# Kernel optimization log

Hardware: AMD Instinct MI355X
Metric: run time of the kernel (lower is better)

The kernel has to match this reference:

```python
import jax, jax.numpy as jnp
import numpy as np

B, X, Y, Z = 2, 64, 64, 48
T_IN, T_OUT = 10, 20
WIDTH = 20
G = 4              # number of fields / groups
M1 = M2 = M3 = 8   # fourier modes
L = 4              # layers
ORDER = [[0, 1, 2, 3], [1, 2, 3, 0], [2, 3, 0, 1], [3, 0, 1, 2]]
CIN = WIDTH * 4    # mWidth_input_parameters[i] == 4
COUT = WIDTH       # nWidth_output_parameters[i] == 1
EPS = 1e-5


def setup_inputs() -> dict:
    key = jax.random.key(0)
    ks = jax.random.split(key, 12)
    s = 0.02
    return {
        "x": jax.random.normal(ks[0], (B, X, Y, Z, G * T_IN), jnp.float32),
        "p_w": jax.random.normal(ks[1], (G, T_IN + 3, WIDTH), jnp.float32) * s,
        "p_b": jnp.zeros((G, WIDTH), jnp.float32),
        # complex spectral weights stored as (..., 2) = (real, imag); 4 corner blocks
        "spec_w": jax.random.normal(ks[2], (L, G, 4, CIN, COUT, M1, M2, M3, 2), jnp.float32) * (1.0 / CIN),
        "mlp_w1": jax.random.normal(ks[3], (L, G, COUT, COUT), jnp.float32) * s,
        "mlp_b1": jnp.zeros((L, G, COUT), jnp.float32),
        "mlp_w2": jax.random.normal(ks[4], (L, G, COUT, COUT), jnp.float32) * s,
        "mlp_b2": jnp.zeros((L, G, COUT), jnp.float32),
        "w_w": jax.random.normal(ks[5], (L, G, COUT, CIN), jnp.float32) * s,
        "w_b": jnp.zeros((L, G, COUT), jnp.float32),
        "q_w1": jax.random.normal(ks[6], (G, 4 * COUT, COUT), jnp.float32) * s,
        "q_b1": jnp.zeros((G, 4 * COUT), jnp.float32),
        "q_w2": jax.random.normal(ks[7], (G, T_OUT, 4 * COUT), jnp.float32) * s,
        "q_b2": jnp.zeros((G, T_OUT), jnp.float32),
    }


def _instance_norm(v):  # (B,C,X,Y,Z); InstanceNorm3d, affine=False
    m = v.mean(axis=(-3, -2, -1), keepdims=True)
    var = v.var(axis=(-3, -2, -1), keepdims=True)
    return (v - m) * jax.lax.rsqrt(var + EPS)


def _conv1x1(v, w, b):  # w: (Co, Ci)
    return jnp.einsum('bixyz,oi->boxyz', v, w) + b[None, :, None, None, None]


def _gelu(v):
    return jax.nn.gelu(v, approximate=False)


def _spectral(v, w):  # v: (B,Ci,X,Y,Z); w: complex (4,Ci,Co,M1,M2,M3)
    ft = jnp.fft.rfftn(v, axes=(-3, -2, -1))
    mul = lambda xc, wc: jnp.einsum('bixyz,ioxyz->boxyz', xc, wc)
    out = jnp.zeros((v.shape[0], w.shape[2], X, Y, Z // 2 + 1), ft.dtype)
    out = out.at[:, :, :M1, :M2, :M3].set(mul(ft[:, :, :M1, :M2, :M3], w[0]))
    out = out.at[:, :, -M1:, :M2, :M3].set(mul(ft[:, :, -M1:, :M2, :M3], w[1]))
    out = out.at[:, :, :M1, -M2:, :M3].set(mul(ft[:, :, :M1, -M2:, :M3], w[2]))
    out = out.at[:, :, -M1:, -M2:, :M3].set(mul(ft[:, :, -M1:, -M2:, :M3], w[3]))
    return jnp.fft.irfftn(out, s=(X, Y, Z), axes=(-3, -2, -1))


def _grid():  # (1,X,Y,Z,3), linspace 0..1 per axis
    gx = jnp.linspace(0.0, 1.0, X, dtype=jnp.float32)[:, None, None]
    gy = jnp.linspace(0.0, 1.0, Y, dtype=jnp.float32)[None, :, None]
    gz = jnp.linspace(0.0, 1.0, Z, dtype=jnp.float32)[None, None, :]
    g = jnp.stack([jnp.broadcast_to(gx, (X, Y, Z)),
                   jnp.broadcast_to(gy, (X, Y, Z)),
                   jnp.broadcast_to(gz, (X, Y, Z))], axis=-1)
    return g[None]


def reference(x, p_w, p_b, spec_w, mlp_w1, mlp_b1, mlp_w2, mlp_b2,
              w_w, w_b, q_w1, q_b1, q_w2, q_b2):
    grid = jnp.broadcast_to(_grid(), (x.shape[0], X, Y, Z, 3))
    # --- lifting: per-field Linear(T_in+3 -> width) ---
    lifted = [jnp.concatenate([x[..., i * T_IN:(i + 1) * T_IN], grid], axis=-1) @ p_w[i] + p_b[i]
              for i in range(G)]
    h = jnp.concatenate(lifted, axis=-1).transpose(0, 4, 1, 2, 3)  # (B, width*G, X, Y, Z)
    sw = spec_w[..., 0] + 1j * spec_w[..., 1]
    for l in range(L):
        for i in range(G):
            # faithful gather quirk: first index duplicated, last index dropped
            idx = [ORDER[i][0]] + ORDER[i][:-1]
            xg = jnp.concatenate([h[:, WIDTH * k:WIDTH * (k + 1)] for k in idx], axis=1)
            v = _instance_norm(xg)
            v = _spectral(v, sw[l, i])
            v = _instance_norm(v)
            v = _conv1x1(_gelu(_conv1x1(v, mlp_w1[l, i], mlp_b1[l, i])), mlp_w2[l, i], mlp_b2[l, i])
            r = _conv1x1(xg, w_w[l, i], w_b[l, i])
            h = h.at[:, WIDTH * i:WIDTH * (i + 1)].set(v + r)
        if l != L - 1:
            h = _gelu(h)
    # --- projection: per-field MLP (T_OUT == WIDTH so slices align to field blocks) ---
    outs = []
    for i in range(G):
        lo = (WIDTH if i == 0 else T_OUT) * i
        xi = h[:, lo:lo + WIDTH]
        xi = _conv1x1(_gelu(_conv1x1(xi, q_w1[i], q_b1[i])), q_w2[i], q_b2[i])
        outs.append(xi)
    out = jnp.concatenate(outs, axis=1)
    return out.transpose(0, 2, 3, 4, 1)  # (B,X,Y,Z,G*T_OUT)
```

## Files before the change

kernel.cpp:

```cpp
#include <hip/hip_runtime.h>
#include <math.h>

#define SPAT 196608
#define EPSV 1e-5f

__device__ __forceinline__ float geluf(float x){
    return 0.5f*x*(1.0f + erff(x*0.70710678118654752440f));
}
__device__ __forceinline__ float wred(float v){
    #pragma unroll
    for(int o=32;o>0;o>>=1) v += __shfl_down(v,o);
    return v;
}

__global__ void k_tables(float* tab){
    for(int idx=threadIdx.x; idx<384; idx+=blockDim.x){
        int z = idx>>3, k = idx&7;
        double a = 6.283185307179586476925286766559 * (double)((k*z)%48) / 48.0;
        float c = (float)cos(a), s = (float)sin(a);
        tab[idx]=c; tab[384+idx]=s;
        tab[768 + k*48+z]=c; tab[1152 + k*48+z]=s;
    }
    for(int idx=threadIdx.x; idx<1024; idx+=blockDim.x){
        int y = idx>>4, ki = idx&15;
        int ka = ki<8 ? ki : ki+48;
        double a = 6.283185307179586476925286766559 * (double)((ka*y)%64) / 64.0;
        float c=(float)cos(a), s=(float)sin(a);
        tab[1536+idx]=c; tab[2560+idx]=s;
        tab[3584 + ki*64+y]=c; tab[4608 + ki*64+y]=s;
    }
}

__global__ void __launch_bounds__(256) k_lift(const float* __restrict__ x,
                       const float* __restrict__ pw, const float* __restrict__ pb,
                       float* __restrict__ h){
    int t = blockIdx.x*256 + threadIdx.x;
    int b = (t>=SPAT) ? 1 : 0; int col = t - b*SPAT;
    int xy = col/48, z = col%48;
    const float4* xp = (const float4*)(x + (size_t)t*40);
    float in[40];
    #pragma unroll
    for(int q=0;q<10;q++){
        float4 v = xp[q];
        in[q*4]=v.x; in[q*4+1]=v.y; in[q*4+2]=v.z; in[q*4+3]=v.w;
    }
    float gx = (float)(xy>>6)*(1.0f/63.0f);
    float gy = (float)(xy&63)*(1.0f/63.0f);
    float gz = (float)z*(1.0f/47.0f);
    for(int g=0;g<4;g++){
        const float* w = pw + g*260;
        #pragma unroll 4
        for(int c=0;c<20;c++){
            float a = pb[g*20+c];
            #pragma unroll
            for(int j=0;j<10;j++) a += in[g*10+j]*w[j*20+c];
            a += gx*w[200+c] + gy*w[220+c] + gz*w[240+c];
            h[(size_t)(b*80+g*20+c)*SPAT + col] = a;
        }
    }
}

__global__ void __launch_bounds__(256) k_zy(const float* __restrict__ h,
        float* __restrict__ ybuf, float* __restrict__ partZY,
        const float* __restrict__ tab, int gA,int gB,int gC,int gD){
    __shared__ __align__(16) float hl[64*52];
    __shared__ float sp[16*65];
    __shared__ float cyl[16*65], syl[16*65];
    __shared__ float sred[8];
    int blk = blockIdx.x;
    int x = blk&63; int d=(blk>>6)%20; int r2 = blk/1280; int b = r2&1; int gi = r2>>1;
    int gl4[4]={gA,gB,gC,gD};
    int g = gl4[gi];
    int ch = g*20+d;
    int tid=threadIdx.x;
    const float4* src = (const float4*)(h + (size_t)(b*80+ch)*SPAT + (size_t)x*3072);
    float s1=0,s2=0;
    #pragma unroll
    for(int u=0;u<3;u++){
        int e=tid+u*256; float4 v=src[e];
        int y=e/12, zq=e%12;
        *(float4*)(hl + y*52 + zq*4) = v;
        s1 += v.x+v.y+v.z+v.w; s2 += v.x*v.x+v.y*v.y+v.z*v.z+v.w*v.w;
    }
    for(int tt=tid;tt<1024;tt+=256){
        int ki=tt>>6, y=tt&63;
        cyl[ki*65+y]=tab[3584+tt]; syl[ki*65+y]=tab[4608+tt];
    }
    s1=wred(s1); s2=wred(s2);
    if((tid&63)==0){ sred[(tid>>6)*2]=s1; sred[(tid>>6)*2+1]=s2; }
    __syncthreads();
    if(tid==0){
        size_t pi = ((size_t)(b*80+ch)*64+x)*2;
        partZY[pi]   = sred[0]+sred[2]+sred[4]+sred[6];
        partZY[pi+1] = sred[1]+sred[3]+sred[5]+sred[7];
    }
    {
        int y = tid&63; int kq = tid>>6;
        float v[48];
        const float4* hr4 = (const float4*)(hl + y*52);
        #pragma unroll
        for(int q=0;q<12;q++){
            float4 t4=hr4[q];
            v[q*4]=t4.x; v[q*4+1]=t4.y; v[q*4+2]=t4.z; v[q*4+3]=t4.w;
        }
        #pragma unroll
        for(int kk=0;kk<2;kk++){
            int k = kq*2+kk;
            const float* CZ = tab+768+k*48;
            const float* SZ = tab+1152+k*48;
            float rr=0, si=0;
            #pragma unroll
            for(int z=0;z<48;z++){ rr += v[z]*CZ[z]; si += v[z]*SZ[z]; }
            sp[(k*2)*65+y]=rr; sp[(k*2+1)*65+y]=-si;
        }
    }
    __syncthreads();
    if(tid<128){
        int ky=tid>>3, kz=tid&7;
        const float* cy = cyl+ky*65; const float* sy = syl+ky*65;
        const float* spr = sp + (kz*2)*65;
        const float* spi = sp + (kz*2+1)*65;
        float fr=0, fi=0;
        #pragma unroll 8
        for(int y=0;y<64;y++){
            float sr=spr[y], si=spi[y];
            float c=cy[y], s=sy[y];
            fr += sr*c + si*s;
            fi += si*c - sr*s;
        }
        size_t base = ((size_t)((g*2+b)*20+d)*16 + ky)*1024 + (size_t)(kz*128);
        ybuf[base + x]      = fr;
        ybuf[base + 64 + x] = fi;
    }
}

__global__ void __launch_bounds__(128) k_xdft(const float* __restrict__ ybuf,
        float* __restrict__ fbufC, const float* __restrict__ partZY,
        const float* __restrict__ tab, int gA,int gB,int gC,int gD){
    __shared__ __align__(16) float ylx[16*68];
    __shared__ float cxl[16*65], sxl[16*65];
    __shared__ float scs[1];
    int blk = blockIdx.x;
    int kyi = blk&15; int d=(blk>>4)%20; int r2=blk/320; int b=r2&1; int gi=r2>>1;
    int gl4[4]={gA,gB,gC,gD};
    int g=gl4[gi]; int ch=g*20+d;
    int tid=threadIdx.x;
    const float4* src = (const float4*)(ybuf + (((size_t)((g*2+b)*20+d)*16+kyi)*1024));
    #pragma unroll
    for(int u=0;u<2;u++){
        int e=tid+u*128; float4 v=src[e];
        int kzri = e>>4; int xx=(e&15)*4;
        *(float4*)(ylx + kzri*68 + xx) = v;
    }
    for(int tt=tid;tt<1024;tt+=128){
        int ki=tt>>6, y=tt&63;
        cxl[ki*65+y]=tab[3584+tt]; sxl[ki*65+y]=tab[4608+tt];
    }
    float s1=0,s2=0;
    if(tid<64){
        size_t pi=((size_t)(b*80+ch)*64+tid)*2;
        s1=partZY[pi]; s2=partZY[pi+1];
    }
    s1=wred(s1); s2=wred(s2);
    if(tid==0){
        float mean=s1*(1.0f/196608.0f);
        float var=s2*(1.0f/196608.0f)-mean*mean;
        scs[0]=rsqrtf(var+EPSV);
    }
    __syncthreads();
    float sc = scs[0];
    int kxi=tid>>3, kz=tid&7;
    const float* yr = ylx + (kz*2)*68;
    const float* yi = ylx + (kz*2+1)*68;
    const float* cx = cxl + kxi*65;
    const float* sx = sxl + kxi*65;
    float fr=0, fi=0;
    #pragma unroll 8
    for(int xx=0;xx<64;xx++){
        float a=yr[xx], e2=yi[xx];
        float c=cx[xx], s=sx[xx];
        fr += a*c + e2*s;
        fi += e2*c - a*s;
    }
    fr*=sc; fi*=sc;
    if(kxi==0 && kyi==0 && kz==0){ fr=0.0f; fi=0.0f; }
    size_t idx = ((size_t)(b*80+ch)*2048 + (size_t)((kxi*16+kyi)*8+kz))*2;
    fbufC[idx]=fr; fbufC[idx+1]=fi;
}

__global__ void __launch_bounds__(256) k_res(const float* __restrict__ h,
        const float* __restrict__ ww, const float* __restrict__ wb,
        float* __restrict__ rbuf, int li, int g0, int g1, int g2){
    int t = blockIdx.x*256 + threadIdx.x;
    int b = t/49152; int r = t - b*49152; int xy = r/12; int zq = r%12;
    const float* W = ww + li*1600;
    float4 acc[20];
    #pragma unroll
    for(int o=0;o<20;o++){ float bv = wb[li*20+o]; acc[o]=make_float4(bv,bv,bv,bv); }
    size_t sp = (size_t)xy*48 + zq*4;
    const float* h0 = h + ((size_t)(b*80+g0*20))*SPAT + sp;
    const float* h1 = h + ((size_t)(b*80+g1*20))*SPAT + sp;
    const float* h2 = h + ((size_t)(b*80+g2*20))*SPAT + sp;
    for(int c=0;c<20;c++){
        float4 v = *(const float4*)(h0 + (size_t)c*SPAT);
        #pragma unroll
        for(int o=0;o<20;o++){
            float w = W[o*80+c] + W[o*80+20+c];
            acc[o].x += w*v.x; acc[o].y += w*v.y; acc[o].z += w*v.z; acc[o].w += w*v.w;
        }
    }
    for(int c=0;c<20;c++){
        float4 v = *(const float4*)(h1 + (size_t)c*SPAT);
        #pragma unroll
        for(int o=0;o<20;o++){
            float w = W[o*80+40+c];
            acc[o].x += w*v.x; acc[o].y += w*v.y; acc[o].z += w*v.z; acc[o].w += w*v.w;
        }
    }
    for(int c=0;c<20;c++){
        float4 v = *(const float4*)(h2 + (size_t)c*SPAT);
        #pragma unroll
        for(int o=0;o<20;o++){
            float w = W[o*80+60+c];
            acc[o].x += w*v.x; acc[o].y += w*v.y; acc[o].z += w*v.z; acc[o].w += w*v.w;
        }
    }
    #pragma unroll
    for(int o=0;o<20;o++)
        *(float4*)(rbuf + ((size_t)(b*20+o))*SPAT + sp) = acc[o];
}

__global__ void k_spec(const float* __restrict__ fbufC, const float* __restrict__ sw,
                       float* __restrict__ gbuf, float* __restrict__ stat2,
                       int li, int g0, int g1, int g2){
    int blk = blockIdx.x;
    int m1p = blk & 3, o = (blk>>2)%20, q = blk/80;
    if(q==0 && m1p==0 && threadIdx.x<2){
        int b = threadIdx.x;
        stat2[(b*20+o)*2]=0.f; stat2[(b*20+o)*2+1]=0.f;
    }
    int offx = (q&1)*8, offy = (q>>1)*8;
    int t = threadIdx.x;
    int m1 = m1p*2 + (t>>5);
    int m2 = (t>>2)&7;
    int m3 = (t&3)*2;
    int tw = m1*64 + m2*8 + m3;
    int kxi = m1+offx, kyi = m2+offy;
    int fo = (kxi*16 + kyi)*8 + m3;
    const float4* wp = (const float4*)(sw + (((size_t)(li*4+q)*1600) + o)*1024 + (size_t)tw*2);
    const float4* fb = (const float4*)fbufC + (fo>>1);
    float r00=0,i00=0,r01=0,i01=0, r10=0,i10=0,r11=0,i11=0;
    #pragma unroll 4
    for(int c=0;c<20;c++){
        float4 wa = wp[(size_t)c*5120];
        float4 wb4= wp[(size_t)(c+20)*5120];
        float wr0 = wa.x + wb4.x, wi0 = wa.y + wb4.y, wr1 = wa.z + wb4.z, wi1 = wa.w + wb4.w;
        float4 f0 = fb[(size_t)(g0*20+c)*1024];
        float4 f1 = fb[(size_t)(80+g0*20+c)*1024];
        r00 += f0.x*wr0 - f0.y*wi0; i00 += f0.x*wi0 + f0.y*wr0;
        r01 += f0.z*wr1 - f0.w*wi1; i01 += f0.z*wi1 + f0.w*wr1;
        r10 += f1.x*wr0 - f1.y*wi0; i10 += f1.x*wi0 + f1.y*wr0;
        r11 += f1.z*wr1 - f1.w*wi1; i11 += f1.z*wi1 + f1.w*wr1;
    }
    #pragma unroll 4
    for(int c=0;c<20;c++){
        float4 wa = wp[(size_t)(c+40)*5120];
        float4 f0 = fb[(size_t)(g1*20+c)*1024];
        float4 f1 = fb[(size_t)(80+g1*20+c)*1024];
        r00 += f0.x*wa.x - f0.y*wa.y; i00 += f0.x*wa.y + f0.y*wa.x;
        r01 += f0.z*wa.z - f0.w*wa.w; i01 += f0.z*wa.w + f0.w*wa.z;
        r10 += f1.x*wa.x - f1.y*wa.y; i10 += f1.x*wa.y + f1.y*wa.x;
        r11 += f1.z*wa.z - f1.w*wa.w; i11 += f1.z*wa.w + f1.w*wa.z;
    }
    #pragma unroll 4
    for(int c=0;c<20;c++){
        float4 wa = wp[(size_t)(c+60)*5120];
        float4 f0 = fb[(size_t)(g2*20+c)*1024];
        float4 f1 = fb[(size_t)(80+g2*20+c)*1024];
        r00 += f0.x*wa.x - f0.y*wa.y; i00 += f0.x*wa.y + f0.y*wa.x;
        r01 += f0.z*wa.z - f0.w*wa.w; i01 += f0.z*wa.w + f0.w*wa.z;
        r10 += f1.x*wa.x - f1.y*wa.y; i10 += f1.x*wa.y + f1.y*wa.x;
        r11 += f1.z*wa.z - f1.w*wa.w; i11 += f1.z*wa.w + f1.w*wa.z;
    }
    float4* gg0 = (float4*)(gbuf + (size_t)o*4096 + fo*2);
    float4* gg1 = (float4*)(gbuf + (size_t)(20+o)*4096 + fo*2);
    *gg0 = make_float4(r00,i00,r01,i01);
    *gg1 = make_float4(r10,i10,r11,i11);
}

__global__ void k_inv(const float* __restrict__ gbuf, float* __restrict__ iybuf,
                      float* __restrict__ stat2, const float* __restrict__ tab){
    __shared__ __align__(16) float gl[4096];
    __shared__ float tmp[256];
    __shared__ float cl[1088], sl[1088];
    __shared__ float ig[4];
    int blk = blockIdx.x;
    int nx = blk&63, o = (blk>>6)%20, b = blk/1280;
    const float4* src4 = (const float4*)(gbuf + (size_t)(b*20+o)*4096);
    for(int t=threadIdx.x;t<1024;t+=blockDim.x) ((float4*)gl)[t]=src4[t];
    for(int t=threadIdx.x;t<1024;t+=blockDim.x){
        int y=t>>4, ki=t&15;
        cl[y*17+ki]=tab[1536+t]; sl[y*17+ki]=tab[2560+t];
    }
    __syncthreads();
    {
        int kyi = threadIdx.x>>3, kz = threadIdx.x&7;
        float ar=0, ai=0;
        #pragma unroll 4
        for(int kxi=0;kxi<16;kxi++){
            float gr = gl[((kxi*16+kyi)*8+kz)*2], gi2 = gl[((kxi*16+kyi)*8+kz)*2+1];
            float c = cl[nx*17+kxi], s = sl[nx*17+kxi];
            ar += gr*c - gi2*s;
            ai += gi2*c + gr*s;
        }
        tmp[threadIdx.x*2]   = ar*(1.0f/64.0f);
        tmp[threadIdx.x*2+1] = ai*(1.0f/64.0f);
    }
    __syncthreads();
    float p1=0,p2=0;
    for(int j=0;j<4;j++){
        int out = threadIdx.x + j*128;
        int ny = out>>3, kz = out&7;
        float ar=0, ai=0;
        #pragma unroll 4
        for(int kyi=0;kyi<16;kyi++){
            float vr = tmp[(kyi*8+kz)*2], vi = tmp[(kyi*8+kz)*2+1];
            float c = cl[ny*17+kyi], s = sl[ny*17+kyi];
            ar += vr*c - vi*s;
            ai += vi*c + vr*s;
        }
        ar *= (1.0f/64.0f); ai *= (1.0f/64.0f);
        size_t idx = ((((size_t)(b*20+o)*64+nx)*64+ny)*8+kz)*2;
        iybuf[idx]=ar; iybuf[idx+1]=ai;
        if(kz==0){ p1 += ar; p2 += ar*ar; }
        else p2 += 2.0f*(ar*ar+ai*ai);
    }
    p2 *= (1.0f/48.0f);
    float r1=wred(p1), r2=wred(p2);
    int wv = threadIdx.x>>6;
    if((threadIdx.x&63)==0){ ig[wv*2]=r1; ig[wv*2+1]=r2; }
    __syncthreads();
    if(threadIdx.x==0){
        atomicAdd(&stat2[(b*20+o)*2],   ig[0]+ig[2]);
        atomicAdd(&stat2[(b*20+o)*2+1], ig[1]+ig[3]);
    }
}

__global__ void __launch_bounds__(256) k_passD(
        const float* __restrict__ iybuf, const float* __restrict__ rbuf,
        const float* __restrict__ w1, const float* __restrict__ b1,
        const float* __restrict__ w2, const float* __restrict__ b2,
        float* __restrict__ h,
        const float* __restrict__ stat2, const float* __restrict__ tab,
        int li, int grp){
    __shared__ __align__(16) float dl[2560];
    __shared__ __align__(16) float vl[20*392];
    __shared__ float m2l[20], s2l[20];
    __shared__ float czl[384], szl[384];
    int blk = blockIdx.x;
    int nyt = blk&7, nx=(blk>>3)&63, b = blk>>9;
    int tid = threadIdx.x;
    for(int u=tid; u<640; u+=256){
        int o = u>>5, j = u&31;
        const float4* s4 = (const float4*)(iybuf + ((((size_t)(b*20+o)*64+nx)*64 + nyt*8)*16));
        ((float4*)dl)[o*32+j] = s4[j];
    }
    if(tid<20){
        float S1 = stat2[(b*20+tid)*2], S2 = stat2[(b*20+tid)*2+1];
        float mean = S1*(1.0f/196608.0f);
        float var = S2*(1.0f/196608.0f) - mean*mean;
        m2l[tid]=mean; s2l[tid]=rsqrtf(var+EPSV);
    }
    for(int t=tid;t<384;t+=256){ czl[t]=tab[768+t]; szl[t]=tab[1152+t]; }
    __syncthreads();
    for(int idx=tid; idx<7680; idx+=256){
        int o = idx/384, p = idx%384;
        int ny = p/48, nz = p%48;
        const float* dd = dl + o*128 + ny*16;
        float acc = dd[0];
        #pragma unroll
        for(int k=1;k<8;k++)
            acc += 2.0f*(dd[k*2]*czl[k*48+nz] - dd[k*2+1]*szl[k*48+nz]);
        float xv = acc*(1.0f/48.0f);
        vl[o*392+p] = (xv - m2l[o])*s2l[o];
    }
    __syncthreads();
    const float* W1 = w1 + li*400;
    const float* W2 = w2 + li*400;
    const float* B1 = b1 + li*20;
    const float* B2 = b2 + li*20;
    for(int p=tid; p<384; p+=256){
        float vj[20], t1[20];
        #pragma unroll
        for(int j2=0;j2<20;j2++) vj[j2]=vl[j2*392+p];
        #pragma unroll
        for(int oo=0;oo<20;oo++){
            float a = B1[oo];
            #pragma unroll
            for(int j2=0;j2<20;j2++) a += vj[j2]*W1[oo*20+j2];
            t1[oo] = geluf(a);
        }
        #pragma unroll
        for(int oo=0;oo<20;oo++){
            float a = B2[oo];
            #pragma unroll
            for(int j2=0;j2<20;j2++) a += t1[j2]*W2[oo*20+j2];
            vl[oo*392+p] = a;
        }
    }
    __syncthreads();
    int sb = (nx*64 + nyt*8)*48;
    if(tid<240){
        int o = tid/12, s = tid%12;
        const float4* vo4 = (const float4*)(vl + o*392);
        const float4* rb4 = (const float4*)(rbuf + (size_t)(b*20+o)*SPAT + sb);
        float4* hp4 = (float4*)(h + (size_t)(b*80+grp*20+o)*SPAT + sb);
        #pragma unroll
        for(int j=0;j<8;j++){
            int qq = s + j*12;
            float4 v = vo4[qq], r = rb4[qq];
            v.x+=r.x; v.y+=r.y; v.z+=r.z; v.w+=r.w;
            hp4[qq]=v;
        }
    }
}

__global__ void k_gelu(float* __restrict__ h){
    int blk = blockIdx.x;
    size_t base = (size_t)blk*4096;
    float4* hp = (float4*)(h+base);
    for(int e=threadIdx.x;e<1024;e+=blockDim.x){
        float4 v = hp[e];
        v.x=geluf(v.x); v.y=geluf(v.y); v.z=geluf(v.z); v.w=geluf(v.w);
        hp[e]=v;
    }
}

__global__ void __launch_bounds__(256) k_head(const float* __restrict__ h,
        const float* __restrict__ qw1, const float* __restrict__ qb1,
        const float* __restrict__ qw2, const float* __restrict__ qb2,
        float* __restrict__ out){
    int g = blockIdx.x & 3;
    int t = (blockIdx.x>>2)*256 + threadIdx.x;
    int b = (t>=SPAT) ? 1 : 0; int col = t - b*SPAT;
    const float* hb = h + (size_t)(b*80+g*20)*SPAT + col;
    float in20[20];
    #pragma unroll
    for(int j=0;j<20;j++) in20[j] = hb[(size_t)j*SPAT];
    float o20[20];
    #pragma unroll
    for(int o2=0;o2<20;o2++) o20[o2] = qb2[g*20+o2];
    for(int o8=0;o8<80;o8++){
        float a = qb1[g*80+o8];
        #pragma unroll
        for(int j=0;j<20;j++) a += in20[j]*qw1[g*1600 + o8*20 + j];
        a = geluf(a);
        #pragma unroll
        for(int o2=0;o2<20;o2++) o20[o2] += a*qw2[g*1600 + o2*80 + o8];
    }
    float* op = out + (size_t)t*80 + g*20;
    #pragma unroll
    for(int q=0;q<5;q++)
        *(float4*)(op + q*4) = make_float4(o20[q*4],o20[q*4+1],o20[q*4+2],o20[q*4+3]);
}

extern "C" void kernel_launch(void* const* d_in, const int* in_sizes, int n_in,
                              void* d_out, int out_size, void* d_ws, size_t ws_size,
                              hipStream_t stream){
    (void)in_sizes; (void)n_in; (void)out_size;
    const float* x    = (const float*)d_in[0];
    const float* p_w  = (const float*)d_in[1];
    const float* p_b  = (const float*)d_in[2];
    const float* spec = (const float*)d_in[3];
    const float* w1   = (const float*)d_in[4];
    const float* b1   = (const float*)d_in[5];
    const float* w2   = (const float*)d_in[6];
    const float* b2   = (const float*)d_in[7];
    const float* ww   = (const float*)d_in[8];
    const float* wb   = (const float*)d_in[9];
    const float* qw1  = (const float*)d_in[10];
    const float* qb1  = (const float*)d_in[11];
    const float* qw2  = (const float*)d_in[12];
    const float* qb2  = (const float*)d_in[13];
    float* out = (float*)d_out;
    float* ws  = (float*)d_ws;

    if(ws_size < (size_t)45409872*4) return;

    float* h      = ws;
    float* rbuf   = ws + 31457280;
    float* ybuf   = ws + 39321600;
    float* gbuf   = ws + 41943040;
    float* iyb    = ws + 42106880;
    float* fbufC  = ws + 44728320;
    float* partZY = ws + 45383680;
    float* stat2  = ws + 45404160;
    float* tab    = ws + 45404240;

    k_tables<<<1,256,0,stream>>>(tab);
    k_lift<<<1536,256,0,stream>>>(x, p_w, p_b, h);

    static const int ORD3[4][3] = {{0,1,2},{1,2,3},{2,3,0},{3,0,1}};
    for(int l=0;l<4;l++){
        for(int bi=0;bi<2;bi++){
            if(bi==0){
                k_zy  <<<10240,256,0,stream>>>(h, ybuf, partZY, tab, 0,1,2,3);
                k_xdft<<< 2560,128,0,stream>>>(ybuf, fbufC, partZY, tab, 0,1,2,3);
            } else {
                k_zy  <<< 5120,256,0,stream>>>(h, ybuf, partZY, tab, 0,1,0,0);
                k_xdft<<< 1280,128,0,stream>>>(ybuf, fbufC, partZY, tab, 0,1,0,0);
            }
            for(int ii=0;ii<2;ii++){
                int i = bi*2+ii; int li = l*4+i;
                int g0=ORD3[i][0], g1=ORD3[i][1], g2=ORD3[i][2];
                k_res  <<< 384,256,0,stream>>>(h, ww, wb, rbuf, li, g0,g1,g2);
                k_spec <<< 320, 64,0,stream>>>(fbufC, spec, gbuf, stat2, li, g0,g1,g2);
                k_inv  <<<2560,128,0,stream>>>(gbuf, iyb, stat2, tab);
                k_passD<<<1024,256,0,stream>>>(iyb, rbuf, w1, b1, w2, b2, h, stat2, tab, li, i);
            }
        }
        if(l<3) k_gelu<<<7680,256,0,stream>>>(h);
    }
    k_head<<<6144,256,0,stream>>>(h, qw1, qb1, qw2, qb2, out);
}
```

Baseline: 3.566 ms.

## Fuse residual conv into passD, split spec channels across threads, widen head

The separate k_res kernel is removed, and the 1x1 residual convolution is computed inside k_passD from h. It is added to the spectral/MLP result, which eliminates the rbuf write and read and one launch per group. k_spec now uses 256 threads that split the 20-channel reduction four ways, with a shared-memory partial-sum combine to improve parallelism. k_head processes two spatial points per thread with half the blocks. The risk is heavier per-thread register use in k_passD and a read of h while the same group's output slice is written in place. g0 equals grp for every group, so the fused path reads the correct inputs.

```diff
diff --git a/kernel.cpp b/kernel.cpp
--- a/kernel.cpp
+++ b/kernel.cpp
@@ -188,70 +188,31 @@
     fbufC[idx]=fr; fbufC[idx+1]=fi;
 }
 
-__global__ void __launch_bounds__(256) k_res(const float* __restrict__ h,
-        const float* __restrict__ ww, const float* __restrict__ wb,
-        float* __restrict__ rbuf, int li, int g0, int g1, int g2){
-    int t = blockIdx.x*256 + threadIdx.x;
-    int b = t/49152; int r = t - b*49152; int xy = r/12; int zq = r%12;
-    const float* W = ww + li*1600;
-    float4 acc[20];
-    #pragma unroll
-    for(int o=0;o<20;o++){ float bv = wb[li*20+o]; acc[o]=make_float4(bv,bv,bv,bv); }
-    size_t sp = (size_t)xy*48 + zq*4;
-    const float* h0 = h + ((size_t)(b*80+g0*20))*SPAT + sp;
-    const float* h1 = h + ((size_t)(b*80+g1*20))*SPAT + sp;
-    const float* h2 = h + ((size_t)(b*80+g2*20))*SPAT + sp;
-    for(int c=0;c<20;c++){
-        float4 v = *(const float4*)(h0 + (size_t)c*SPAT);
-        #pragma unroll
-        for(int o=0;o<20;o++){
-            float w = W[o*80+c] + W[o*80+20+c];
-            acc[o].x += w*v.x; acc[o].y += w*v.y; acc[o].z += w*v.z; acc[o].w += w*v.w;
-        }
-    }
-    for(int c=0;c<20;c++){
-        float4 v = *(const float4*)(h1 + (size_t)c*SPAT);
-        #pragma unroll
-        for(int o=0;o<20;o++){
-            float w = W[o*80+40+c];
-            acc[o].x += w*v.x; acc[o].y += w*v.y; acc[o].z += w*v.z; acc[o].w += w*v.w;
-        }
-    }
-    for(int c=0;c<20;c++){
-        float4 v = *(const float4*)(h2 + (size_t)c*SPAT);
-        #pragma unroll
-        for(int o=0;o<20;o++){
-            float w = W[o*80+60+c];
-            acc[o].x += w*v.x; acc[o].y += w*v.y; acc[o].z += w*v.z; acc[o].w += w*v.w;
-        }
-    }
-    #pragma unroll
-    for(int o=0;o<20;o++)
-        *(float4*)(rbuf + ((size_t)(b*20+o))*SPAT + sp) = acc[o];
-}
-
-__global__ void k_spec(const float* __restrict__ fbufC, const float* __restrict__ sw,
-                       float* __restrict__ gbuf, float* __restrict__ stat2,
-                       int li, int g0, int g1, int g2){
+__global__ void __launch_bounds__(256) k_spec(const float* __restrict__ fbufC,
+        const float* __restrict__ sw, float* __restrict__ gbuf,
+        float* __restrict__ stat2, int li, int g0, int g1, int g2){
+    __shared__ float part[2112];
     int blk = blockIdx.x;
     int m1p = blk & 3, o = (blk>>2)%20, q = blk/80;
-    if(q==0 && m1p==0 && threadIdx.x<2){
-        int b = threadIdx.x;
-        stat2[(b*20+o)*2]=0.f; stat2[(b*20+o)*2+1]=0.f;
+    int tid = threadIdx.x;
+    int t64 = tid & 63, cc = tid >> 6;
+    if(q==0 && m1p==0 && tid<2){
+        stat2[(tid*20+o)*2]=0.f; stat2[(tid*20+o)*2+1]=0.f;
     }
     int offx = (q&1)*8, offy = (q>>1)*8;
-    int t = threadIdx.x;
-    int m1 = m1p*2 + (t>>5);
-    int m2 = (t>>2)&7;
-    int m3 = (t&3)*2;
+    int m1 = m1p*2 + (t64>>5);
+    int m2 = (t64>>2)&7;
+    int m3 = (t64&3)*2;
     int tw = m1*64 + m2*8 + m3;
     int kxi = m1+offx, kyi = m2+offy;
     int fo = (kxi*16 + kyi)*8 + m3;
     const float4* wp = (const float4*)(sw + (((size_t)(li*4+q)*1600) + o)*1024 + (size_t)tw*2);
     const float4* fb = (const float4*)fbufC + (fo>>1);
     float r00=0,i00=0,r01=0,i01=0, r10=0,i10=0,r11=0,i11=0;
-    #pragma unroll 4
-    for(int c=0;c<20;c++){
+    int c0 = cc*5;
+    #pragma unroll
+    for(int u=0;u<5;u++){
+        int c = c0+u;
         float4 wa = wp[(size_t)c*5120];
         float4 wb4= wp[(size_t)(c+20)*5120];
         float wr0 = wa.x + wb4.x, wi0 = wa.y + wb4.y, wr1 = wa.z + wb4.z, wi1 = wa.w + wb4.w;
@@ -262,8 +223,9 @@
         r10 += f1.x*wr0 - f1.y*wi0; i10 += f1.x*wi0 + f1.y*wr0;
         r11 += f1.z*wr1 - f1.w*wi1; i11 += f1.z*wi1 + f1.w*wr1;
     }
-    #pragma unroll 4
-    for(int c=0;c<20;c++){
+    #pragma unroll
+    for(int u=0;u<5;u++){
+        int c = c0+u;
         float4 wa = wp[(size_t)(c+40)*5120];
         float4 f0 = fb[(size_t)(g1*20+c)*1024];
         float4 f1 = fb[(size_t)(80+g1*20+c)*1024];
@@ -272,8 +234,9 @@
         r10 += f1.x*wa.x - f1.y*wa.y; i10 += f1.x*wa.y + f1.y*wa.x;
         r11 += f1.z*wa.z - f1.w*wa.w; i11 += f1.z*wa.w + f1.w*wa.z;
     }
-    #pragma unroll 4
-    for(int c=0;c<20;c++){
+    #pragma unroll
+    for(int u=0;u<5;u++){
+        int c = c0+u;
         float4 wa = wp[(size_t)(c+60)*5120];
         float4 f0 = fb[(size_t)(g2*20+c)*1024];
         float4 f1 = fb[(size_t)(80+g2*20+c)*1024];
@@ -282,10 +245,22 @@
         r10 += f1.x*wa.x - f1.y*wa.y; i10 += f1.x*wa.y + f1.y*wa.x;
         r11 += f1.z*wa.z - f1.w*wa.w; i11 += f1.z*wa.w + f1.w*wa.z;
     }
-    float4* gg0 = (float4*)(gbuf + (size_t)o*4096 + fo*2);
-    float4* gg1 = (float4*)(gbuf + (size_t)(20+o)*4096 + fo*2);
-    *gg0 = make_float4(r00,i00,r01,i01);
-    *gg1 = make_float4(r10,i10,r11,i11);
+    float vals[8]={r00,i00,r01,i01,r10,i10,r11,i11};
+    #pragma unroll
+    for(int e=0;e<8;e++) part[t64*33 + e*4 + cc] = vals[e];
+    __syncthreads();
+    if(cc==0){
+        float acc[8];
+        #pragma unroll
+        for(int e=0;e<8;e++){
+            const float* p = part + t64*33 + e*4;
+            acc[e] = p[0]+p[1]+p[2]+p[3];
+        }
+        float4* gg0 = (float4*)(gbuf + (size_t)o*4096 + fo*2);
+        float4* gg1 = (float4*)(gbuf + (size_t)(20+o)*4096 + fo*2);
+        *gg0 = make_float4(acc[0],acc[1],acc[2],acc[3]);
+        *gg1 = make_float4(acc[4],acc[5],acc[6],acc[7]);
+    }
 }
 
 __global__ void k_inv(const float* __restrict__ gbuf, float* __restrict__ iybuf,
@@ -347,12 +322,13 @@
 }
 
 __global__ void __launch_bounds__(256) k_passD(
-        const float* __restrict__ iybuf, const float* __restrict__ rbuf,
+        const float* __restrict__ iybuf,
         const float* __restrict__ w1, const float* __restrict__ b1,
         const float* __restrict__ w2, const float* __restrict__ b2,
+        const float* __restrict__ ww, const float* __restrict__ wb,
         float* __restrict__ h,
         const float* __restrict__ stat2, const float* __restrict__ tab,
-        int li, int grp){
+        int li, int grp, int g1, int g2){
     __shared__ __align__(16) float dl[2560];
     __shared__ __align__(16) float vl[20*392];
     __shared__ float m2l[20], s2l[20];
@@ -410,17 +386,41 @@
     }
     __syncthreads();
     int sb = (nx*64 + nyt*8)*48;
-    if(tid<240){
-        int o = tid/12, s = tid%12;
-        const float4* vo4 = (const float4*)(vl + o*392);
-        const float4* rb4 = (const float4*)(rbuf + (size_t)(b*20+o)*SPAT + sb);
-        float4* hp4 = (float4*)(h + (size_t)(b*80+grp*20+o)*SPAT + sb);
-        #pragma unroll
-        for(int j=0;j<8;j++){
-            int qq = s + j*12;
-            float4 v = vo4[qq], r = rb4[qq];
-            v.x+=r.x; v.y+=r.y; v.z+=r.z; v.w+=r.w;
-            hp4[qq]=v;
+    if(tid<192){
+        const float* W = ww + li*1600;
+        float2 acc[20];
+        #pragma unroll
+        for(int o=0;o<20;o++){ float bv = wb[li*20+o]; acc[o].x=bv; acc[o].y=bv; }
+        const float* hb = h + (size_t)(b*80)*SPAT + sb + tid*2;
+        for(int c=0;c<20;c++){
+            float2 v = *(const float2*)(hb + (size_t)(grp*20+c)*SPAT);
+            #pragma unroll
+            for(int o=0;o<20;o++){
+                float w = W[o*80+c] + W[o*80+20+c];
+                acc[o].x += w*v.x; acc[o].y += w*v.y;
+            }
+        }
+        for(int c=0;c<20;c++){
+            float2 v = *(const float2*)(hb + (size_t)(g1*20+c)*SPAT);
+            #pragma unroll
+            for(int o=0;o<20;o++){
+                float w = W[o*80+40+c];
+                acc[o].x += w*v.x; acc[o].y += w*v.y;
+            }
+        }
+        for(int c=0;c<20;c++){
+            float2 v = *(const float2*)(hb + (size_t)(g2*20+c)*SPAT);
+            #pragma unroll
+            for(int o=0;o<20;o++){
+                float w = W[o*80+60+c];
+                acc[o].x += w*v.x; acc[o].y += w*v.y;
+            }
+        }
+        #pragma unroll
+        for(int o=0;o<20;o++){
+            float2 mv = *(const float2*)(vl + o*392 + tid*2);
+            float2 r; r.x = mv.x + acc[o].x; r.y = mv.y + acc[o].y;
+            *(float2*)(h + (size_t)(b*80+grp*20+o)*SPAT + sb + tid*2) = r;
         }
     }
 }
@@ -442,26 +442,37 @@
         float* __restrict__ out){
     int g = blockIdx.x & 3;
     int t = (blockIdx.x>>2)*256 + threadIdx.x;
-    int b = (t>=SPAT) ? 1 : 0; int col = t - b*SPAT;
+    if(t >= 196608) return;
+    int b = (t>=98304) ? 1 : 0; int col = (t - b*98304)*2;
     const float* hb = h + (size_t)(b*80+g*20)*SPAT + col;
-    float in20[20];
-    #pragma unroll
-    for(int j=0;j<20;j++) in20[j] = hb[(size_t)j*SPAT];
-    float o20[20];
-    #pragma unroll
-    for(int o2=0;o2<20;o2++) o20[o2] = qb2[g*20+o2];
+    float2 in20[20];
+    #pragma unroll
+    for(int j=0;j<20;j++) in20[j] = *(const float2*)(hb + (size_t)j*SPAT);
+    float2 o20[20];
+    #pragma unroll
+    for(int o2=0;o2<20;o2++){ float bv = qb2[g*20+o2]; o20[o2].x=bv; o20[o2].y=bv; }
     for(int o8=0;o8<80;o8++){
-        float a = qb1[g*80+o8];
-        #pragma unroll
-        for(int j=0;j<20;j++) a += in20[j]*qw1[g*1600 + o8*20 + j];
-        a = geluf(a);
-        #pragma unroll
-        for(int o2=0;o2<20;o2++) o20[o2] += a*qw2[g*1600 + o2*80 + o8];
-    }
-    float* op = out + (size_t)t*80 + g*20;
-    #pragma unroll
-    for(int q=0;q<5;q++)
-        *(float4*)(op + q*4) = make_float4(o20[q*4],o20[q*4+1],o20[q*4+2],o20[q*4+3]);
+        float bv = qb1[g*80+o8];
+        float a0 = bv, a1 = bv;
+        #pragma unroll
+        for(int j=0;j<20;j++){
+            float w = qw1[g*1600 + o8*20 + j];
+            a0 += in20[j].x*w; a1 += in20[j].y*w;
+        }
+        a0 = geluf(a0); a1 = geluf(a1);
+        #pragma unroll
+        for(int o2=0;o2<20;o2++){
+            float w = qw2[g*1600 + o2*80 + o8];
+            o20[o2].x += a0*w; o20[o2].y += a1*w;
+        }
+    }
+    float* op0 = out + ((size_t)(b*SPAT)+col)*80 + g*20;
+    float* op1 = op0 + 80;
+    #pragma unroll
+    for(int q2=0;q2<5;q2++){
+        *(float4*)(op0 + q2*4) = make_float4(o20[q2*4].x,o20[q2*4+1].x,o20[q2*4+2].x,o20[q2*4+3].x);
+        *(float4*)(op1 + q2*4) = make_float4(o20[q2*4].y,o20[q2*4+1].y,o20[q2*4+2].y,o20[q2*4+3].y);
+    }
 }
 
 extern "C" void kernel_launch(void* const* d_in, const int* in_sizes, int n_in,
@@ -485,17 +496,16 @@
     float* out = (float*)d_out;
     float* ws  = (float*)d_ws;
 
-    if(ws_size < (size_t)45409872*4) return;
+    if(ws_size < (size_t)37545552*4) return;
 
     float* h      = ws;
-    float* rbuf   = ws + 31457280;
-    float* ybuf   = ws + 39321600;
-    float* gbuf   = ws + 41943040;
-    float* iyb    = ws + 42106880;
-    float* fbufC  = ws + 44728320;
-    float* partZY = ws + 45383680;
-    float* stat2  = ws + 45404160;
-    float* tab    = ws + 45404240;
+    float* ybuf   = ws + 31457280;
+    float* gbuf   = ws + 34078720;
+    float* iyb    = ws + 34242560;
+    float* fbufC  = ws + 36864000;
+    float* partZY = ws + 37519360;
+    float* stat2  = ws + 37539840;
+    float* tab    = ws + 37539920;
 
     k_tables<<<1,256,0,stream>>>(tab);
     k_lift<<<1536,256,0,stream>>>(x, p_w, p_b, h);
@@ -513,13 +523,13 @@
             for(int ii=0;ii<2;ii++){
                 int i = bi*2+ii; int li = l*4+i;
                 int g0=ORD3[i][0], g1=ORD3[i][1], g2=ORD3[i][2];
-                k_res  <<< 384,256,0,stream>>>(h, ww, wb, rbuf, li, g0,g1,g2);
-                k_spec <<< 320, 64,0,stream>>>(fbufC, spec, gbuf, stat2, li, g0,g1,g2);
+                (void)g0;
+                k_spec <<< 320,256,0,stream>>>(fbufC, spec, gbuf, stat2, li, g0,g1,g2);
                 k_inv  <<<2560,128,0,stream>>>(gbuf, iyb, stat2, tab);
-                k_passD<<<1024,256,0,stream>>>(iyb, rbuf, w1, b1, w2, b2, h, stat2, tab, li, i);
+                k_passD<<<1024,256,0,stream>>>(iyb, w1, b1, w2, b2, ww, wb, h, stat2, tab, li, i, g1, g2);
             }
         }
         if(l<3) k_gelu<<<7680,256,0,stream>>>(h);
     }
-    k_head<<<6144,256,0,stream>>>(h, qw1, qb1, qw2, qb2, out);
-}
+    k_head<<<3072,256,0,stream>>>(h, qw1, qb1, qw2, qb2, out);
+}
```

New measurement: 3.379 ms. 1.06x faster.
